# Kernel tuning notes

Measured on AMD Instinct MI355X. Metric: run time of the kernel, lower is better.

Reference implementation:

```python
import jax, jax.numpy as jnp
import numpy as np

DIM = 96
HID = 384
DEPTH = 5
HEADS = 8
INNER = 64 * DIM          # inner_dim = dim_head * dim per source (dim_head=64)
DH = INNER // HEADS       # per-head dim = 768
SCALE = 64 ** -0.5        # scale uses default dim_head=64, not actual per-head dim
EPS = 1e-5


def setup_inputs() -> dict:
    key = jax.random.key(0)
    ks = jax.random.split(key, 13)
    def p(k, shape, s=0.02):
        return jax.random.normal(k, shape, jnp.float32) * s
    return {
        "x": jax.random.normal(ks[0], (2, 512, DIM), jnp.float32),
        "gam_a": p(ks[1], (DEPTH, 3, DIM)),          # attention pre-norm gammas
        "Wq": p(ks[2], (DEPTH, 3, DIM, INNER)),
        "Wk": p(ks[3], (DEPTH, 3, DIM, INNER)),
        "Wv": p(ks[4], (DEPTH, 3, DIM, INNER)),
        "Wo": p(ks[5], (DEPTH, 3, INNER, DIM)),
        "gam_m": p(ks[6], (DEPTH, 2, DIM)),          # MLP pre-norm gammas
        "W1": p(ks[7], (DEPTH, 2, DIM, HID)),
        "b1": p(ks[8], (DEPTH, 2, HID)),
        "W2": p(ks[9], (DEPTH, 2, HID, DIM)),
        "b2": p(ks[10], (DEPTH, 2, DIM)),
        "gam_mid": p(ks[11], (DEPTH, DIM)),          # bare LayerNorm inside each block
        "gam_final": p(ks[12], (DIM,)),
    }


def _ln(x, g):
    # nn.LayerNorm(elementwise_affine=False) followed by x * (gamma + 1)
    mu = x.mean(-1, keepdims=True)
    var = ((x - mu) ** 2).mean(-1, keepdims=True)
    return (x - mu) * jax.lax.rsqrt(var + EPS) * (g + 1.0)


def _attn(x, g, wq, wk, wv, wo):
    b, n, _ = x.shape
    h = _ln(x, g)                                    # self.norm (reuse_attention=True)
    q = (h @ wq).reshape(b, n, HEADS, DH).transpose(0, 2, 1, 3) * SCALE
    k = (h @ wk).reshape(b, n, HEADS, DH).transpose(0, 2, 1, 3)
    v = (h @ wv).reshape(b, n, HEADS, DH).transpose(0, 2, 1, 3)
    sim = jnp.einsum("bhid,bhjd->bhij", q, k)        # [b,h,n,n]
    a = jax.nn.softmax(sim, axis=-1)                 # dropout=0.0 -> identity
    o = jnp.einsum("bhij,bhjd->bhid", a, v)
    return o.transpose(0, 2, 1, 3).reshape(b, n, INNER) @ wo


def _mlp(x, g, w1, b1_, w2, b2_):
    # LayerNorm -> Linear -> GELU(exact) -> Linear (dropouts eval-mode identity)
    h = jax.nn.gelu(_ln(x, g) @ w1 + b1_, approximate=False)
    return h @ w2 + b2_


def reference(x, gam_a, Wq, Wk, Wv, Wo, gam_m, W1, b1, W2, b2, gam_mid, gam_final):
    for d in range(DEPTH):
        x = _attn(x, gam_a[d, 0], Wq[d, 0], Wk[d, 0], Wv[d, 0], Wo[d, 0]) + x
        x = _mlp(x, gam_m[d, 0], W1[d, 0], b1[d, 0], W2[d, 0], b2[d, 0]) + x
        x = _attn(x, gam_a[d, 1], Wq[d, 1], Wk[d, 1], Wv[d, 1], Wo[d, 1]) + x
        x = _attn(x, gam_a[d, 2], Wq[d, 2], Wk[d, 2], Wv[d, 2], Wo[d, 2]) + x
        x = _ln(x, gam_mid[d])                       # bare LayerNorm, NO residual
        x = _mlp(x, gam_m[d, 1], W1[d, 1], b1[d, 1], W2[d, 1], b2[d, 1]) + x
    return _ln(x, gam_final)
```

## Files before the change

### kernel.cpp

```cpp
#include <hip/hip_runtime.h>
#include <hip/hip_bf16.h>

typedef __hip_bfloat16 bf16;
typedef __attribute__((ext_vector_type(8))) short bf16x8;
typedef __attribute__((ext_vector_type(4))) float f32x4;

#define TOK    1024
#define DIM    96
#define HIDN   384
#define HEADS  8
#define DH     768
#define INNER  6144
#define SEQ    512
#define NDEPTH 5
#define EPSLN  1e-5f
#define QSCALE 0.125f

#define MFMA16(a, b, c) __builtin_amdgcn_mfma_f32_16x16x32_bf16((a), (b), (c), 0, 0, 0)

__device__ __forceinline__ float b2f(bf16 v) { return __bfloat162float(v); }
__device__ __forceinline__ bf16  f2b(float v) { return __float2bfloat16(v); }

__device__ __forceinline__ float gload(const void* p, size_t i, int f) {
  return f ? b2f(((const bf16*)p)[i]) : ((const float*)p)[i];
}
__device__ __forceinline__ const char* gptr(const void* base, size_t off, int f) {
  return (const char*)base + off * (size_t)(f ? 2 : 4);
}

__device__ __forceinline__ uint4 pack8(float4 u0, float4 u1) {
  alignas(16) unsigned short o[8];
  bf16 t;
  t = f2b(u0.x); o[0] = *(unsigned short*)&t;
  t = f2b(u0.y); o[1] = *(unsigned short*)&t;
  t = f2b(u0.z); o[2] = *(unsigned short*)&t;
  t = f2b(u0.w); o[3] = *(unsigned short*)&t;
  t = f2b(u1.x); o[4] = *(unsigned short*)&t;
  t = f2b(u1.y); o[5] = *(unsigned short*)&t;
  t = f2b(u1.z); o[6] = *(unsigned short*)&t;
  t = f2b(u1.w); o[7] = *(unsigned short*)&t;
  return *(const uint4*)o;
}

__global__ __launch_bounds__(256) void detect_kernel(const void* xraw, int* flag) {
  __shared__ int cnt[256];
  int t = threadIdx.x;
  const unsigned short* u = (const unsigned short*)xraw;
  int c = 0;
  #pragma unroll
  for (int i = 0; i < 4; i++) {
    unsigned short h = u[2 * (t * 4 + i)];
    int e = (h >> 7) & 0xFF;
    if (e >= 87 && e <= 132) c++;
  }
  cnt[t] = c;
  __syncthreads();
  for (int s = 128; s > 0; s >>= 1) {
    if (t < s) cnt[t] += cnt[t + s];
    __syncthreads();
  }
  if (t == 0) *flag = (cnt[0] > 700) ? 1 : 0;
}

__global__ __launch_bounds__(256) void wtrans_kernel(
    const void* __restrict__ src, int R, int C,
    bf16* __restrict__ dst, const int* __restrict__ flagp) {
  __shared__ float tile[32][65];
  int f = *flagp;
  int t = threadIdx.x;
  int c0 = blockIdx.x * 64, r0 = blockIdx.y * 32;
  size_t bb = (size_t)blockIdx.z * R * C;
  int ty = t >> 4, tx = t & 15;
  #pragma unroll
  for (int half = 0; half < 2; half++) {
    int r = r0 + ty + half * 16;
    int c = c0 + tx * 4;
    if (c < C) {
      size_t idx = bb + (size_t)r * C + c;
      float v0, v1, v2, v3;
      if (f) {
        uint2 u = *(const uint2*)((const unsigned short*)src + idx);
        v0 = __uint_as_float((u.x & 0xffffu) << 16);
        v1 = __uint_as_float(u.x & 0xffff0000u);
        v2 = __uint_as_float((u.y & 0xffffu) << 16);
        v3 = __uint_as_float(u.y & 0xffff0000u);
      } else {
        float4 v = *(const float4*)((const float*)src + idx);
        v0 = v.x; v1 = v.y; v2 = v.z; v3 = v.w;
      }
      tile[ty + half * 16][tx * 4 + 0] = v0;
      tile[ty + half * 16][tx * 4 + 1] = v1;
      tile[ty + half * 16][tx * 4 + 2] = v2;
      tile[ty + half * 16][tx * 4 + 3] = v3;
    }
  }
  __syncthreads();
  int cc = c0 + (t >> 2), rseg = (t & 3) * 8;
  if (cc < C) {
    int cs = cc - c0;
    alignas(16) unsigned short o[8];
    #pragma unroll
    for (int j = 0; j < 8; j++) {
      bf16 tv = f2b(tile[rseg + j][cs]);
      o[j] = *(unsigned short*)&tv;
    }
    *(uint4*)&dst[bb + (size_t)cc * R + r0 + rseg] = *(const uint4*)o;
  }
}

template <int WM>
__device__ __forceinline__ void gemm_bt_body(
    const void* __restrict__ A, int aF32, int lda,
    const void* __restrict__ Bt, int bF32, int ldb,
    int m0, int n0, int kbeg, int kend, int Mtot, int N,
    float alpha, bf16* __restrict__ Cb, int ldc) {
  constexpr int TM = WM * 32;
  __shared__ bf16 As[TM][40];
  __shared__ bf16 Bs[128][40];
  int t = threadIdx.x;
  int lane = t & 63;
  int wave = t >> 6;
  int wm = (wave >> 1) * (WM * 16), wn = (wave & 1) * 64;
  f32x4 acc[WM][4];
  #pragma unroll
  for (int i = 0; i < WM; i++)
    #pragma unroll
    for (int j = 0; j < 4; j++) acc[i][j] = (f32x4){0.f, 0.f, 0.f, 0.f};

  int arow = t >> 2, aseg = (t & 3) * 8;

  for (int kb = kbeg; kb < kend; kb += 32) {
    #pragma unroll
    for (int i = 0; i < (TM + 63) / 64; i++) {
      int rr = arow + i * 64;
      if ((TM % 64 == 0) || rr < TM) {
        int gm = min(m0 + rr, Mtot - 1);
        size_t idx = (size_t)gm * lda + kb + aseg;
        if (aF32) {
          const float* Af = (const float*)A;
          float4 u0 = *(const float4*)(Af + idx);
          float4 u1 = *(const float4*)(Af + idx + 4);
          *(uint4*)&As[rr][aseg] = pack8(u0, u1);
        } else {
          *(uint4*)&As[rr][aseg] = *(const uint4*)((const bf16*)A + idx);
        }
      }
    }
    #pragma unroll
    for (int i = 0; i < 2; i++) {
      int r = arow + i * 64;
      int gn = n0 + r;
      if (gn < N) {
        size_t idx = (size_t)gn * ldb + kb + aseg;
        if (bF32) {
          const float* Bf = (const float*)Bt;
          float4 u0 = *(const float4*)(Bf + idx);
          float4 u1 = *(const float4*)(Bf + idx + 4);
          *(uint4*)&Bs[r][aseg] = pack8(u0, u1);
        } else {
          *(uint4*)&Bs[r][aseg] = *(const uint4*)((const bf16*)Bt + idx);
        }
      } else {
        uint4 zz = {0, 0, 0, 0};
        *(uint4*)&Bs[r][aseg] = zz;
      }
    }
    __syncthreads();
    int fm = lane & 15, fq = (lane >> 4) * 8;
    bf16x8 af[WM], bfv[4];
    #pragma unroll
    for (int i = 0; i < WM; i++)
      af[i] = *(const bf16x8*)&As[wm + i * 16 + fm][fq];
    #pragma unroll
    for (int j = 0; j < 4; j++)
      bfv[j] = *(const bf16x8*)&Bs[wn + j * 16 + fm][fq];
    #pragma unroll
    for (int i = 0; i < WM; i++)
      #pragma unroll
      for (int j = 0; j < 4; j++)
        acc[i][j] = MFMA16(af[i], bfv[j], acc[i][j]);
    __syncthreads();
  }
  int col = lane & 15, rq = (lane >> 4) * 4;
  #pragma unroll
  for (int j = 0; j < 4; j++) {
    int gn = n0 + wn + j * 16 + col;
    if (gn >= N) continue;
    #pragma unroll
    for (int i = 0; i < WM; i++) {
      #pragma unroll
      for (int r = 0; r < 4; r++) {
        int gm = m0 + wm + i * 16 + rq + r;
        if (gm >= Mtot) continue;
        Cb[(size_t)gm * ldc + gn] = f2b(acc[i][j][r] * alpha);
      }
    }
  }
}

__global__ __launch_bounds__(256) void mtgt_kernel(
    const void* __restrict__ WqE, const void* __restrict__ WkE,
    const void* __restrict__ WvE, const bf16* __restrict__ woT,
    bf16* __restrict__ Mt, bf16* __restrict__ Gt,
    const int* __restrict__ flagp) {
  int f = *flagp;
  int z = blockIdx.z;
  bool isM = z < 120;
  int zz = isM ? z : z - 120;
  int L = zz >> 3, h = zz & 7;
  size_t wo = (size_t)L * DIM * INNER + (size_t)h * DH;
  size_t wo2 = f ? wo : wo;
  const void* A  = isM ? (const void*)((const char*)WkE + wo2 * (f ? 2 : 4))
                       : (const void*)(woT + wo);
  const void* Bt = isM ? (const void*)((const char*)WqE + wo2 * (f ? 2 : 4))
                       : (const void*)((const char*)WvE + wo2 * (f ? 2 : 4));
  int aF32 = isM ? !f : 0;
  int bF32 = !f;
  bf16* C = (isM ? Mt : Gt) + (size_t)zz * DIM * DIM;
  gemm_bt_body<3>(A, aF32, INNER, Bt, bF32, INNER, 0, 0, 0, DH, DIM, DIM,
                  isM ? QSCALE : 1.f, C, DIM);
}

__device__ __forceinline__ void ln_row_vals(float v0, float v1in, int lane,
    const char* g, int f, float& o0, float& o1) {
  float v1 = (lane < 32) ? v1in : 0.f;
  float s = v0 + v1;
  #pragma unroll
  for (int off = 32; off > 0; off >>= 1) s += __shfl_xor(s, off);
  float mu = s * (1.f / 96.f);
  float d0 = v0 - mu;
  float d1 = (lane < 32) ? (v1 - mu) : 0.f;
  float q = d0 * d0 + d1 * d1;
  #pragma unroll
  for (int off = 32; off > 0; off >>= 1) q += __shfl_xor(q, off);
  float rstd = rsqrtf(q * (1.f / 96.f) + EPSLN);
  o0 = d0 * rstd * (gload(g, lane, f) + 1.f);
  o1 = (lane < 32) ? (d1 * rstd * (gload(g, 64 + lane, f) + 1.f)) : 0.f;
}

__device__ __forceinline__ void store_hn(bf16* hn, bf16* hnT, int row, int lane,
                                         float o0, float o1) {
  size_t base = (size_t)row * DIM;
  bf16* hT = hnT + (size_t)(row >> 9) * DIM * SEQ;
  int ss = row & (SEQ - 1);
  hn[base + lane] = f2b(o0);
  hT[(size_t)lane * SEQ + ss] = f2b(o0);
  if (lane < 32) {
    hn[base + 64 + lane] = f2b(o1);
    hT[(size_t)(64 + lane) * SEQ + ss] = f2b(o1);
  }
}

__global__ __launch_bounds__(256) void castln_kernel(
    const void* __restrict__ in_x, float* __restrict__ x,
    bf16* __restrict__ hn, bf16* __restrict__ hnT,
    const void* __restrict__ gb, const int* __restrict__ flagp) {
  int f = *flagp;
  int wave = threadIdx.x >> 6, lane = threadIdx.x & 63;
  int row = blockIdx.x * 4 + wave;
  size_t base = (size_t)row * DIM;
  float v0 = gload(in_x, base + lane, f);
  float v1 = (lane < 32) ? gload(in_x, base + 64 + lane, f) : 0.f;
  x[base + lane] = v0;
  if (lane < 32) x[base + 64 + lane] = v1;
  float o0, o1;
  ln_row_vals(v0, v1, lane, gptr(gb, 0, f), f, o0, o1);
  store_hn(hn, hnT, row, lane, o0, o1);
}

__global__ __launch_bounds__(256) void ln_kernel(
    const float* __restrict__ x, bf16* __restrict__ hn, bf16* __restrict__ hnT,
    const void* __restrict__ gb, size_t goff, const int* __restrict__ flagp) {
  int f = *flagp;
  int wave = threadIdx.x >> 6, lane = threadIdx.x & 63;
  int row = blockIdx.x * 4 + wave;
  size_t base = (size_t)row * DIM;
  float v0 = x[base + lane];
  float v1 = (lane < 32) ? x[base + 64 + lane] : 0.f;
  float o0, o1;
  ln_row_vals(v0, v1, lane, gptr(gb, goff, f), f, o0, o1);
  store_hn(hn, hnT, row, lane, o0, o1);
}

__global__ __launch_bounds__(512) void fattn4_kernel(
    const bf16* __restrict__ hn,
    const bf16* __restrict__ hnT,
    const bf16* __restrict__ MtL,
    const bf16* __restrict__ GtL,
    float* __restrict__ x) {
  __shared__ bf16 tP[32][520];
  __shared__ bf16 Zs[32][104];
  __shared__ float red[2][8][32];
  int tid = threadIdx.x, lane = tid & 63, wave = tid >> 6;
  int fm = lane & 15, fq = (lane >> 4) * 8;
  int col = lane & 15, rq = (lane >> 4) * 4;
  int z = blockIdx.y, b = z >> 3, h = z & 7;
  int m0 = blockIdx.x * 32;
  const bf16* hnB = hn + (size_t)b * SEQ * DIM;
  const bf16* hTB = hnT + (size_t)b * DIM * SEQ;
  const bf16* MtH = MtL + (size_t)h * DIM * DIM;
  const bf16* GtH = GtL + (size_t)h * DIM * DIM;

  if (wave < 6) {
    int mA = wave & 1, nb = wave >> 1;
    f32x4 a0 = (f32x4){0.f, 0.f, 0.f, 0.f}, a1 = a0;
    #pragma unroll
    for (int kb = 0; kb < 96; kb += 32) {
      bf16x8 af = *(const bf16x8*)(hnB + (size_t)(m0 + mA * 16 + fm) * DIM + kb + fq);
      bf16x8 b0 = *(const bf16x8*)(MtH + (size_t)(nb * 16 + fm) * DIM + kb + fq);
      bf16x8 b1 = *(const bf16x8*)(MtH + (size_t)((nb + 3) * 16 + fm) * DIM + kb + fq);
      a0 = MFMA16(af, b0, a0);
      a1 = MFMA16(af, b1, a1);
    }
    #pragma unroll
    for (int r = 0; r < 4; r++) {
      Zs[mA * 16 + rq + r][nb * 16 + col] = f2b(a0[r]);
      Zs[mA * 16 + rq + r][(nb + 3) * 16 + col] = f2b(a1[r]);
    }
  }
  __syncthreads();

  f32x4 acc2[2][4];
  #pragma unroll
  for (int i = 0; i < 2; i++)
    #pragma unroll
    for (int j = 0; j < 4; j++) acc2[i][j] = (f32x4){0.f, 0.f, 0.f, 0.f};
  #pragma unroll
  for (int kb = 0; kb < 96; kb += 32) {
    bf16x8 af0 = *(const bf16x8*)&Zs[fm][kb + fq];
    bf16x8 af1 = *(const bf16x8*)&Zs[16 + fm][kb + fq];
    bf16x8 bv[4];
    #pragma unroll
    for (int j = 0; j < 4; j++)
      bv[j] = *(const bf16x8*)(hnB + (size_t)(wave * 64 + j * 16 + fm) * DIM + kb + fq);
    #pragma unroll
    for (int j = 0; j < 4; j++) {
      acc2[0][j] = MFMA16(af0, bv[j], acc2[0][j]);
      acc2[1][j] = MFMA16(af1, bv[j], acc2[1][j]);
    }
  }

  float rmax[2][4];
  #pragma unroll
  for (int i = 0; i < 2; i++)
    #pragma unroll
    for (int r = 0; r < 4; r++) {
      float m = -1e30f;
      #pragma unroll
      for (int j = 0; j < 4; j++) m = fmaxf(m, acc2[i][j][r]);
      rmax[i][r] = m;
    }
  #pragma unroll
  for (int s = 1; s < 16; s <<= 1)
    #pragma unroll
    for (int i = 0; i < 2; i++)
      #pragma unroll
      for (int r = 0; r < 4; r++)
        rmax[i][r] = fmaxf(rmax[i][r], __shfl_xor(rmax[i][r], s));
  if (col == 0)
    #pragma unroll
    for (int i = 0; i < 2; i++)
      #pragma unroll
      for (int r = 0; r < 4; r++) red[0][wave][i * 16 + rq + r] = rmax[i][r];
  __syncthreads();
  float rsum[2][4];
  #pragma unroll
  for (int i = 0; i < 2; i++)
    #pragma unroll
    for (int r = 0; r < 4; r++) {
      int row = i * 16 + rq + r;
      float gm = red[0][0][row];
      #pragma unroll
      for (int q = 1; q < 8; q++) gm = fmaxf(gm, red[0][q][row]);
      float s = 0.f;
      #pragma unroll
      for (int j = 0; j < 4; j++) {
        float e = __expf(acc2[i][j][r] - gm);
        acc2[i][j][r] = e;
        s += e;
      }
      rsum[i][r] = s;
    }
  #pragma unroll
  for (int s = 1; s < 16; s <<= 1)
    #pragma unroll
    for (int i = 0; i < 2; i++)
      #pragma unroll
      for (int r = 0; r < 4; r++)
        rsum[i][r] += __shfl_xor(rsum[i][r], s);
  if (col == 0)
    #pragma unroll
    for (int i = 0; i < 2; i++)
      #pragma unroll
      for (int r = 0; r < 4; r++) red[1][wave][i * 16 + rq + r] = rsum[i][r];
  __syncthreads();

  #pragma unroll
  for (int i = 0; i < 2; i++)
    #pragma unroll
    for (int r = 0; r < 4; r++) {
      int row = i * 16 + rq + r;
      float tot = red[1][0][row];
      #pragma unroll
      for (int q = 1; q < 8; q++) tot += red[1][q][row];
      float inv = 1.f / tot;
      #pragma unroll
      for (int j = 0; j < 4; j++)
        tP[row][wave * 64 + j * 16 + col] = f2b(acc2[i][j][r] * inv);
    }
  __syncthreads();

  f32x4 z0 = (f32x4){0.f, 0.f, 0.f, 0.f}, z1 = z0;
  if (wave < 4) {
    int n = wave;
    #pragma unroll 4
    for (int kb = 0; kb < 512; kb += 32) {
      bf16x8 bv = *(const bf16x8*)(hTB + (size_t)(n * 16 + fm) * SEQ + kb + fq);
      bf16x8 af0 = *(const bf16x8*)&tP[fm][kb + fq];
      bf16x8 af1 = *(const bf16x8*)&tP[16 + fm][kb + fq];
      z0 = MFMA16(af0, bv, z0);
      z1 = MFMA16(af1, bv, z1);
    }
    #pragma unroll
    for (int r = 0; r < 4; r++) {
      Zs[rq + r][n * 16 + col] = f2b(z0[r]);
      Zs[16 + rq + r][n * 16 + col] = f2b(z1[r]);
    }
  } else {
    int mA = wave & 1, n = (wave >> 1) + 2;
    #pragma unroll 4
    for (int kb = 0; kb < 512; kb += 32) {
      bf16x8 bv = *(const bf16x8*)(hTB + (size_t)(n * 16 + fm) * SEQ + kb + fq);
      bf16x8 af = *(const bf16x8*)&tP[mA * 16 + fm][kb + fq];
      z0 = MFMA16(af, bv, z0);
    }
    #pragma unroll
    for (int r = 0; r < 4; r++)
      Zs[mA * 16 + rq + r][n * 16 + col] = f2b(z0[r]);
  }
  __syncthreads();

  if (wave < 6) {
    int mA = wave & 1, nb = wave >> 1;
    f32x4 o0 = (f32x4){0.f, 0.f, 0.f, 0.f}, o1 = o0;
    #pragma unroll
    for (int kb = 0; kb < 96; kb += 32) {
      bf16x8 af = *(const bf16x8*)&Zs[mA * 16 + fm][kb + fq];
      bf16x8 b0 = *(const bf16x8*)(GtH + (size_t)(nb * 16 + fm) * DIM + kb + fq);
      bf16x8 b1 = *(const bf16x8*)(GtH + (size_t)((nb + 3) * 16 + fm) * DIM + kb + fq);
      o0 = MFMA16(af, b0, o0);
      o1 = MFMA16(af, b1, o1);
    }
    #pragma unroll
    for (int r = 0; r < 4; r++) {
      int gr = b * SEQ + m0 + mA * 16 + rq + r;
      atomicAdd(x + (size_t)gr * DIM + nb * 16 + col, o0[r]);
      atomicAdd(x + (size_t)gr * DIM + (nb + 3) * 16 + col, o1[r]);
    }
  }
}

__global__ __launch_bounds__(512) void fmlp_kernel(
    float* __restrict__ X,
    const void* __restrict__ gmidb, size_t gmidoff, int useMid,
    const void* __restrict__ gmb, size_t gmoff,
    const bf16* __restrict__ w1T,
    const void* __restrict__ b1b, size_t b1off,
    const bf16* __restrict__ w2T,
    const void* __restrict__ b2b, size_t b2off,
    int lnmode, const void* __restrict__ lngb, size_t lngoff,
    bf16* __restrict__ hn, bf16* __restrict__ hnT, void* __restrict__ dout,
    const int* __restrict__ flagp) {
  __shared__ float X1s[32][96];
  __shared__ bf16 As[32][104];
  __shared__ bf16 Hs[32][392];
  int f = *flagp;
  int tid = threadIdx.x, lane = tid & 63, wave = tid >> 6;
  int fm = lane & 15, fq = (lane >> 4) * 8;
  int col = lane & 15, rq = (lane >> 4) * 4;
  int m0 = blockIdx.x * 32;
  const char* gm = gptr(gmb, gmoff, f);
  float gm0 = gload(gm, lane, f) + 1.f;
  float gm1 = (lane < 32) ? (gload(gm, 64 + lane, f) + 1.f) : 0.f;
  float gd0 = 1.f, gd1 = 1.f;
  if (useMid) {
    const char* gmid = gptr(gmidb, gmidoff, f);
    gd0 = gload(gmid, lane, f) + 1.f;
    gd1 = (lane < 32) ? (gload(gmid, 64 + lane, f) + 1.f) : 0.f;
  }
  for (int r = wave; r < 32; r += 8) {
    const float* xr = X + (size_t)(m0 + r) * DIM;
    float v0 = xr[lane];
    float v1 = (lane < 32) ? xr[64 + lane] : 0.f;
    if (useMid) {
      float s = v0 + v1;
      #pragma unroll
      for (int off = 32; off > 0; off >>= 1) s += __shfl_xor(s, off);
      float mu = s * (1.f / 96.f);
      float d0 = v0 - mu;
      float d1 = (lane < 32) ? (v1 - mu) : 0.f;
      float q = d0 * d0 + d1 * d1;
      #pragma unroll
      for (int off = 32; off > 0; off >>= 1) q += __shfl_xor(q, off);
      float rstd = rsqrtf(q * (1.f / 96.f) + EPSLN);
      v0 = d0 * rstd * gd0;
      v1 = (lane < 32) ? (d1 * rstd * gd1) : 0.f;
    }
    X1s[r][lane] = v0;
    if (lane < 32) X1s[r][64 + lane] = v1;
    float s = v0 + v1;
    #pragma unroll
    for (int off = 32; off > 0; off >>= 1) s += __shfl_xor(s, off);
    float mu = s * (1.f / 96.f);
    float d0 = v0 - mu;
    float d1 = (lane < 32) ? (v1 - mu) : 0.f;
    float q = d0 * d0 + d1 * d1;
    #pragma unroll
    for (int off = 32; off > 0; off >>= 1) q += __shfl_xor(q, off);
    float rstd = rsqrtf(q * (1.f / 96.f) + EPSLN);
    As[r][lane] = f2b(d0 * rstd * gm0);
    if (lane < 32) As[r][64 + lane] = f2b(d1 * rstd * gm1);
  }
  __syncthreads();

  int mw = wave & 1, nh = wave >> 1;
  f32x4 acc1[6];
  #pragma unroll
  for (int j = 0; j < 6; j++) acc1[j] = (f32x4){0.f, 0.f, 0.f, 0.f};
  #pragma unroll
  for (int kb = 0; kb < 96; kb += 32) {
    bf16x8 af = *(const bf16x8*)&As[mw * 16 + fm][kb + fq];
    #pragma unroll
    for (int j = 0; j < 6; j++) {
      bf16x8 bv = *(const bf16x8*)(w1T + (size_t)(nh * 96 + j * 16 + fm) * DIM + kb + fq);
      acc1[j] = MFMA16(af, bv, acc1[j]);
    }
  }
  const char* b1p = gptr(b1b, b1off, f);
  #pragma unroll
  for (int j = 0; j < 6; j++) {
    int gn = nh * 96 + j * 16 + col;
    float bv = gload(b1p, gn, f);
    #pragma unroll
    for (int r = 0; r < 4; r++) {
      float v = acc1[j][r] + bv;
      v = 0.5f * v * (1.f + erff(v * 0.70710678118f));
      Hs[mw * 16 + rq + r][gn] = f2b(v);
    }
  }
  __syncthreads();

  if (wave < 6) {
    int mA = wave & 1, nb = wave >> 1;
    f32x4 o0 = (f32x4){0.f, 0.f, 0.f, 0.f}, o1 = o0;
    #pragma unroll 4
    for (int kb = 0; kb < 384; kb += 32) {
      bf16x8 af = *(const bf16x8*)&Hs[mA * 16 + fm][kb + fq];
      bf16x8 b0 = *(const bf16x8*)(w2T + (size_t)(nb * 16 + fm) * HIDN + kb + fq);
      bf16x8 b1 = *(const bf16x8*)(w2T + (size_t)((nb + 3) * 16 + fm) * HIDN + kb + fq);
      o0 = MFMA16(af, b0, o0);
      o1 = MFMA16(af, b1, o1);
    }
    const char* b2p = gptr(b2b, b2off, f);
    float bb0 = gload(b2p, nb * 16 + col, f);
    float bb1 = gload(b2p, (nb + 3) * 16 + col, f);
    #pragma unroll
    for (int r = 0; r < 4; r++) {
      int row = mA * 16 + rq + r;
      int gmr = m0 + row;
      float nv0 = X1s[row][nb * 16 + col] + o0[r] + bb0;
      float nv1 = X1s[row][(nb + 3) * 16 + col] + o1[r] + bb1;
      X[(size_t)gmr * DIM + nb * 16 + col] = nv0;
      X[(size_t)gmr * DIM + (nb + 3) * 16 + col] = nv1;
      X1s[row][nb * 16 + col] = nv0;
      X1s[row][(nb + 3) * 16 + col] = nv1;
    }
  }
  __syncthreads();

  const char* lg = gptr(lngb, lngoff, f);
  for (int r = wave; r < 32; r += 8) {
    int row = m0 + r;
    size_t base = (size_t)row * DIM;
    float v0 = X1s[r][lane];
    float v1 = (lane < 32) ? X1s[r][64 + lane] : 0.f;
    float o0, o1;
    ln_row_vals(v0, v1, lane, lg, f, o0, o1);
    if (lnmode == 1) {
      store_hn(hn, hnT, row, lane, o0, o1);
    } else {
      if (!f) {
        ((float*)dout)[base + lane] = o0;
        if (lane < 32) ((float*)dout)[base + 64 + lane] = o1;
      } else {
        ((bf16*)dout)[base + lane] = f2b(o0);
        if (lane < 32) ((bf16*)dout)[base + 64 + lane] = f2b(o1);
      }
    }
  }
}

extern "C" void kernel_launch(void* const* d_in, const int* in_sizes, int n_in,
                              void* d_out, int out_size, void* d_ws, size_t ws_size,
                              hipStream_t stream) {
  const void* in_x    = d_in[0];
  const void* gam_a   = d_in[1];
  const void* Wq      = d_in[2];
  const void* Wk      = d_in[3];
  const void* Wv      = d_in[4];
  const void* Wo      = d_in[5];
  const void* gam_m   = d_in[6];
  const void* W1      = d_in[7];
  const void* b1      = d_in[8];
  const void* W2      = d_in[9];
  const void* b2      = d_in[10];
  const void* gam_mid = d_in[11];
  const void* gam_fin = d_in[12];

  char* wsb = (char*)d_ws;
  size_t off = 0;
  auto carve = [&](size_t bytes) {
    char* p = wsb + off;
    off += (bytes + 255) & ~(size_t)255;
    return p;
  };
  int*   flag = (int*)carve(256);
  float* x    = (float*)carve((size_t)TOK * DIM * 4);
  bf16*  hn   = (bf16*)carve((size_t)TOK * DIM * 2);
  bf16*  hnT  = (bf16*)carve((size_t)2 * DIM * SEQ * 2);
  const size_t WSZ = (size_t)15 * DIM * INNER;
  bf16*  woT  = (bf16*)carve(WSZ * 2);
  bf16*  w1T  = (bf16*)carve((size_t)10 * DIM * HIDN * 2);
  bf16*  w2T  = (bf16*)carve((size_t)10 * DIM * HIDN * 2);
  bf16*  Mt   = (bf16*)carve((size_t)120 * DIM * DIM * 2);
  bf16*  Gt   = (bf16*)carve((size_t)120 * DIM * DIM * 2);

  detect_kernel<<<dim3(1), dim3(256), 0, stream>>>(in_x, flag);

  wtrans_kernel<<<dim3(2, 192, 15), dim3(256), 0, stream>>>(Wo, INNER, DIM, woT, flag);
  wtrans_kernel<<<dim3(6, 3, 10), dim3(256), 0, stream>>>(W1, DIM, HIDN, w1T, flag);
  wtrans_kernel<<<dim3(2, 12, 10), dim3(256), 0, stream>>>(W2, HIDN, DIM, w2T, flag);
  mtgt_kernel<<<dim3(1, 1, 240), dim3(256), 0, stream>>>(
      Wq, Wk, Wv, woT, Mt, Gt, flag);

  castln_kernel<<<dim3(TOK / 4), dim3(256), 0, stream>>>(in_x, x, hn, hnT, gam_a, flag);

  auto attn = [&](int d, int j) {
    size_t gi = ((size_t)d * 3 + j);
    fattn4_kernel<<<dim3(16, 16), dim3(512), 0, stream>>>(
        hn, hnT, Mt + gi * 8 * DIM * DIM, Gt + gi * 8 * DIM * DIM, x);
  };

  for (int d = 0; d < NDEPTH; d++) {
    bool last = (d == NDEPTH - 1);
    attn(d, 0);
    fmlp_kernel<<<dim3(32), dim3(512), 0, stream>>>(
        x, nullptr, 0, 0,
        gam_m, (size_t)(d * 2 + 0) * DIM,
        w1T + (size_t)(d * 2 + 0) * DIM * HIDN, b1, (size_t)(d * 2 + 0) * HIDN,
        w2T + (size_t)(d * 2 + 0) * DIM * HIDN, b2, (size_t)(d * 2 + 0) * DIM,
        1, gam_a, (size_t)(d * 3 + 1) * DIM, hn, hnT, nullptr, flag);
    attn(d, 1);
    ln_kernel<<<dim3(TOK / 4), dim3(256), 0, stream>>>(
        x, hn, hnT, gam_a, (size_t)(d * 3 + 2) * DIM, flag);
    attn(d, 2);
    fmlp_kernel<<<dim3(32), dim3(512), 0, stream>>>(
        x, gam_mid, (size_t)d * DIM, 1,
        gam_m, (size_t)(d * 2 + 1) * DIM,
        w1T + (size_t)(d * 2 + 1) * DIM * HIDN, b1, (size_t)(d * 2 + 1) * HIDN,
        w2T + (size_t)(d * 2 + 1) * DIM * HIDN, b2, (size_t)(d * 2 + 1) * DIM,
        last ? 2 : 1, last ? gam_fin : gam_a,
        last ? (size_t)0 : (size_t)((d + 1) * 3) * DIM,
        hn, hnT, d_out, flag);
  }
}
```

Baseline: 691.0 us.

## Split weight-product GEMM across K halves and M tiles with reduction kernel

The precomputation of per-head Wk^T·Wq and Wo·Wv products now runs as 6 blocks per matrix instead of one: two K-halves times three 32-row M tiles. Each block writes fp32 partials, and a new conversion kernel sums the two halves, applies the query scale and converts to bf16. This targets the low parallelism of launching only 240 blocks, each doing a long serial K loop. In exchange it adds an extra launch and an fp32 partial buffer round trip.

```diff
diff --git a/kernel.cpp b/kernel.cpp
--- a/kernel.cpp
+++ b/kernel.cpp
@@ -113,7 +113,7 @@
     const void* __restrict__ A, int aF32, int lda,
     const void* __restrict__ Bt, int bF32, int ldb,
     int m0, int n0, int kbeg, int kend, int Mtot, int N,
-    float alpha, bf16* __restrict__ Cb, int ldc) {
+    float alpha, bf16* __restrict__ Cb, float* __restrict__ Cf, int ldc) {
   constexpr int TM = WM * 32;
   __shared__ bf16 As[TM][40];
   __shared__ bf16 Bs[128][40];
@@ -192,7 +192,8 @@
       for (int r = 0; r < 4; r++) {
         int gm = m0 + wm + i * 16 + rq + r;
         if (gm >= Mtot) continue;
-        Cb[(size_t)gm * ldc + gn] = f2b(acc[i][j][r] * alpha);
+        if (Cf) Cf[(size_t)gm * ldc + gn] = acc[i][j][r];
+        else    Cb[(size_t)gm * ldc + gn] = f2b(acc[i][j][r] * alpha);
       }
     }
   }
@@ -201,24 +202,44 @@
 __global__ __launch_bounds__(256) void mtgt_kernel(
     const void* __restrict__ WqE, const void* __restrict__ WkE,
     const void* __restrict__ WvE, const bf16* __restrict__ woT,
-    bf16* __restrict__ Mt, bf16* __restrict__ Gt,
-    const int* __restrict__ flagp) {
+    float* __restrict__ P, const int* __restrict__ flagp) {
   int f = *flagp;
   int z = blockIdx.z;
+  int ks = blockIdx.x / 3, mt = blockIdx.x % 3;
   bool isM = z < 120;
   int zz = isM ? z : z - 120;
   int L = zz >> 3, h = zz & 7;
   size_t wo = (size_t)L * DIM * INNER + (size_t)h * DH;
-  size_t wo2 = f ? wo : wo;
-  const void* A  = isM ? (const void*)((const char*)WkE + wo2 * (f ? 2 : 4))
+  const void* A  = isM ? (const void*)((const char*)WkE + wo * (f ? 2 : 4))
                        : (const void*)(woT + wo);
-  const void* Bt = isM ? (const void*)((const char*)WqE + wo2 * (f ? 2 : 4))
-                       : (const void*)((const char*)WvE + wo2 * (f ? 2 : 4));
+  const void* Bt = isM ? (const void*)((const char*)WqE + wo * (f ? 2 : 4))
+                       : (const void*)((const char*)WvE + wo * (f ? 2 : 4));
   int aF32 = isM ? !f : 0;
   int bF32 = !f;
-  bf16* C = (isM ? Mt : Gt) + (size_t)zz * DIM * DIM;
-  gemm_bt_body<3>(A, aF32, INNER, Bt, bF32, INNER, 0, 0, 0, DH, DIM, DIM,
-                  isM ? QSCALE : 1.f, C, DIM);
+  float* Cf = P + ((size_t)ks * 240 + z) * DIM * DIM;
+  gemm_bt_body<1>(A, aF32, INNER, Bt, bF32, INNER,
+                  mt * 32, 0, ks * (DH / 2), (ks + 1) * (DH / 2), DIM, DIM,
+                  1.f, nullptr, Cf, DIM);
+}
+
+__global__ __launch_bounds__(256) void mtcvt_kernel(
+    const float* __restrict__ P, bf16* __restrict__ Mt, bf16* __restrict__ Gt) {
+  const int n = 240 * DIM * DIM;
+  int i0 = (blockIdx.x * 256 + threadIdx.x) * 4;
+  if (i0 >= n) return;
+  int z = i0 / (DIM * DIM);
+  bool isM = z < 120;
+  float alpha = isM ? QSCALE : 1.f;
+  float4 a = *(const float4*)(P + i0);
+  float4 b = *(const float4*)(P + n + i0);
+  bf16* out = isM ? (Mt + i0) : (Gt + (size_t)i0 - (size_t)120 * DIM * DIM);
+  alignas(8) unsigned short o[4];
+  bf16 t;
+  t = f2b((a.x + b.x) * alpha); o[0] = *(unsigned short*)&t;
+  t = f2b((a.y + b.y) * alpha); o[1] = *(unsigned short*)&t;
+  t = f2b((a.z + b.z) * alpha); o[2] = *(unsigned short*)&t;
+  t = f2b((a.w + b.w) * alpha); o[3] = *(unsigned short*)&t;
+  *(uint2*)out = *(const uint2*)o;
 }
 
 __device__ __forceinline__ void ln_row_vals(float v0, float v1in, int lane,
@@ -634,14 +655,16 @@
   bf16*  w2T  = (bf16*)carve((size_t)10 * DIM * HIDN * 2);
   bf16*  Mt   = (bf16*)carve((size_t)120 * DIM * DIM * 2);
   bf16*  Gt   = (bf16*)carve((size_t)120 * DIM * DIM * 2);
+  float* MtP  = (float*)carve((size_t)2 * 240 * DIM * DIM * 4);
 
   detect_kernel<<<dim3(1), dim3(256), 0, stream>>>(in_x, flag);
 
   wtrans_kernel<<<dim3(2, 192, 15), dim3(256), 0, stream>>>(Wo, INNER, DIM, woT, flag);
   wtrans_kernel<<<dim3(6, 3, 10), dim3(256), 0, stream>>>(W1, DIM, HIDN, w1T, flag);
   wtrans_kernel<<<dim3(2, 12, 10), dim3(256), 0, stream>>>(W2, HIDN, DIM, w2T, flag);
-  mtgt_kernel<<<dim3(1, 1, 240), dim3(256), 0, stream>>>(
-      Wq, Wk, Wv, woT, Mt, Gt, flag);
+  mtgt_kernel<<<dim3(6, 1, 240), dim3(256), 0, stream>>>(
+      Wq, Wk, Wv, woT, MtP, flag);
+  mtcvt_kernel<<<dim3(2160), dim3(256), 0, stream>>>(MtP, Mt, Gt);
 
   castln_kernel<<<dim3(TOK / 4), dim3(256), 0, stream>>>(in_x, x, hn, hnT, gam_a, flag);
 
```

Measured after the change: 658.7 us. -4.7%, faster.
